# Performance work log

Hardware: AMD Instinct MI355X
Metric: run time of the kernel (lower is better)

## Reference

```python
import jax, jax.numpy as jnp
import numpy as np

B, T, S, H, NUM_HEAD = 4, 1024, 1024, 1024, 16
CAUSAL = True
EPS = 1e-5            # torch nn.LayerNorm default
NEG = -float(2 ** 32)  # masked_fill value in the source


def setup_inputs() -> dict:
    key = jax.random.key(0)
    ks = jax.random.split(key, 8)
    queries = jax.random.normal(ks[0], (B, T, H), jnp.float32)
    keys = jax.random.normal(ks[1], (B, S, H), jnp.float32)
    queries_mask = jax.random.randint(ks[2], (B, T, 1), 0, 2).astype(jnp.int32)
    keys_mask = jax.random.randint(ks[3], (B, S, 1), 0, 2).astype(jnp.int32)
    Wq = jax.random.normal(ks[4], (H, H), jnp.float32) * 0.02
    Wk = jax.random.normal(ks[5], (H, H), jnp.float32) * 0.02
    Wv = jax.random.normal(ks[6], (H, H), jnp.float32) * 0.02
    bq = jnp.zeros((H,), jnp.float32)
    bk = jnp.zeros((H,), jnp.float32)
    bv = jnp.zeros((H,), jnp.float32)
    gamma = jnp.ones((H,), jnp.float32)
    beta = jnp.zeros((H,), jnp.float32)
    return {"queries": queries, "queries_mask": queries_mask, "keys": keys,
            "keys_mask": keys_mask, "Wq": Wq, "bq": bq, "Wk": Wk, "bk": bk,
            "Wv": Wv, "bv": bv, "gamma": gamma, "beta": beta}


def _layernorm(x, gamma, beta):
    m = jnp.mean(x, axis=-1, keepdims=True)
    v = jnp.mean((x - m) ** 2, axis=-1, keepdims=True)  # biased var, as torch
    return gamma * (x - m) / jnp.sqrt(v + EPS) + beta


def reference(queries, queries_mask, keys, keys_mask, Wq, bq, Wk, bk, Wv, bv, gamma, beta):
    dh = H // NUM_HEAD
    # ReLU-activated QKV projections (torch Linear: x @ W.T + b)
    Q = jax.nn.relu(queries @ Wq.T + bq)            # (B,T,H)
    K = jax.nn.relu(keys @ Wk.T + bk)               # (B,S,H)
    V = jax.nn.relu(keys @ Wv.T + bv)               # (B,S,H)
    # chunk along feature dim then cat along batch == (h, B, L, dh) layout
    Qh = Q.reshape(B, T, NUM_HEAD, dh).transpose(2, 0, 1, 3)
    Kh = K.reshape(B, S, NUM_HEAD, dh).transpose(2, 0, 1, 3)
    Vh = V.reshape(B, S, NUM_HEAD, dh).transpose(2, 0, 1, 3)
    # scaled by sqrt(hidden_size), NOT sqrt(head_dim) — faithful to source
    scores = jnp.einsum('hbtd,hbsd->hbts', Qh, Kh) / float(np.sqrt(H))
    # padding mask via outer product of the two masks
    qm = queries_mask[..., 0].astype(jnp.float32)   # (B,T)
    km = keys_mask[..., 0].astype(jnp.float32)      # (B,S)
    pad = (qm[:, :, None] * km[:, None, :]) == 0.0  # (B,T,S) True -> masked
    scores = jnp.where(pad[None], NEG, scores)
    if CAUSAL:
        tri = jnp.triu(jnp.ones((T, S), bool), k=1)  # triu(ones)-eye == strict upper
        scores = jnp.where(tri[None, None], NEG, scores)
    attn = jax.nn.softmax(scores, axis=-1)
    out = jnp.einsum('hbts,hbsd->hbtd', attn, Vh)   # (h,B,T,dh)
    out = out.transpose(1, 2, 0, 3).reshape(B, T, H)  # cat heads back on feature dim
    out = out * queries_mask.astype(jnp.float32)
    return _layernorm(out + queries, gamma, beta)
```

## Files before the change

kernel.cpp:

```cpp
#include <hip/hip_runtime.h>
#include <hip/hip_bf16.h>
#include <math.h>

#define B_ 4
#define T_ 1024
#define S_ 1024
#define H_ 1024
#define NH_ 16
#define DH_ 64
#define NEGV -4294967296.0f
#define EPS_ 1e-5f

typedef __attribute__((ext_vector_type(8))) short short8;
typedef __attribute__((ext_vector_type(8))) unsigned short ushort8;
typedef __attribute__((ext_vector_type(4))) unsigned short ushort4v;
typedef __attribute__((ext_vector_type(4))) unsigned int uint4v;
typedef __attribute__((ext_vector_type(4))) float f32x4;

__device__ __forceinline__ unsigned short f2bf(float x) {
    unsigned int u = __float_as_uint(x);
    u += 0x7FFF + ((u >> 16) & 1);
    return (unsigned short)(u >> 16);
}

__device__ __forceinline__ float bf2f(unsigned short u) {
    return __uint_as_float(((unsigned int)u) << 16);
}

__device__ __forceinline__ unsigned int pack_bf16(float a, float b) {
    union { __hip_bfloat162 h; unsigned int u; } cv;
    cv.h = __float22bfloat162_rn(float2{a, b});
    return cv.u;
}

__device__ __forceinline__ void gload16(const unsigned short* g, unsigned short* l) {
    __builtin_amdgcn_global_load_lds(
        (const __attribute__((address_space(1))) unsigned int*)g,
        (__attribute__((address_space(3))) unsigned int*)l,
        16, 0, 0);
}

#define VMCNT(n) asm volatile("s_waitcnt vmcnt(" #n ")" ::: "memory")
#define LGKM0()  { asm volatile("s_waitcnt lgkmcnt(0)" ::: "memory"); \
                   __builtin_amdgcn_sched_barrier(0); }

__global__ __launch_bounds__(256) void cast_bf16(
    const float* __restrict__ q, const float* __restrict__ k,
    const float* __restrict__ wq, const float* __restrict__ wk,
    const float* __restrict__ wv,
    unsigned short* __restrict__ dq, unsigned short* __restrict__ dk,
    unsigned short* __restrict__ dwq, unsigned short* __restrict__ dwk,
    unsigned short* __restrict__ dwv)
{
    const int seg = blockIdx.y;
    const float* src; unsigned short* dst; int n;
    switch (seg) {
        case 0:  src = q;  dst = dq;  n = B_*T_*H_; break;
        case 1:  src = k;  dst = dk;  n = B_*S_*H_; break;
        case 2:  src = wq; dst = dwq; n = H_*H_;    break;
        case 3:  src = wk; dst = dwk; n = H_*H_;    break;
        default: src = wv; dst = dwv; n = H_*H_;    break;
    }
    const int i = (blockIdx.x * 256 + threadIdx.x) * 8;
    if (i >= n) return;
    float4 a = *(const float4*)&src[i];
    float4 b = *(const float4*)&src[i + 4];
    ushort8 o;
    o[0] = f2bf(a.x); o[1] = f2bf(a.y); o[2] = f2bf(a.z); o[3] = f2bf(a.w);
    o[4] = f2bf(b.x); o[5] = f2bf(b.y); o[6] = f2bf(b.z); o[7] = f2bf(b.w);
    *(ushort8*)&dst[i] = o;
}

template<int MH, int NH>
__device__ __forceinline__ void mfmaQ(f32x4 (&acc)[8][4],
                                      const short8 (&afr)[4][2],
                                      const short8 (&bfr)[2][2])
{
    #pragma unroll
    for (int i2 = 0; i2 < 4; ++i2)
        #pragma unroll
        for (int j2 = 0; j2 < 2; ++j2)
            #pragma unroll
            for (int kc = 0; kc < 2; ++kc)
                acc[MH*4+i2][NH*2+j2] = __builtin_amdgcn_mfma_f32_16x16x32_bf16(
                    afr[i2][kc], bfr[j2][kc], acc[MH*4+i2][NH*2+j2], 0, 0, 0);
}

__global__ __launch_bounds__(512) void qkv_mfma(
    const unsigned short* __restrict__ Xq, const unsigned short* __restrict__ Xk,
    const unsigned short* __restrict__ Wq, const unsigned short* __restrict__ Wk,
    const unsigned short* __restrict__ Wv,
    const float* __restrict__ bq, const float* __restrict__ bk,
    const float* __restrict__ bv,
    unsigned short* __restrict__ Qo, unsigned short* __restrict__ Ko,
    unsigned short* __restrict__ Vo)
{
    const int bi = (blockIdx.x & 7) * 24 + (blockIdx.x >> 3);
    const int col_t = bi >> 4, row_t = bi & 15;
    const int which = col_t >> 2;
    const int colW = (col_t & 3) * 256;
    const int row0 = row_t * 256;

    const unsigned short* X = (which == 0) ? Xq : Xk;
    const unsigned short* Wm = (which == 0) ? Wq : (which == 1) ? Wk : Wv;
    const float* bias        = (which == 0) ? bq : (which == 1) ? bk : bv;
    unsigned short* Out      = (which == 0) ? Qo : (which == 1) ? Ko : Vo;

    __shared__ __align__(16) unsigned short S[67584];

    const int tid = threadIdx.x;
    const int wid = tid >> 6, lane = tid & 63, lo = lane & 15, hi = lane >> 4;
    const int wm = wid >> 2, wn = wid & 3;
    const int swr = (lo & 7) << 3;
    const int csw = ((tid & 7) << 3) ^ (((tid >> 3) & 7) << 3);

    auto stageA = [&](int mh, int kt) {
        const int k0 = kt << 6;
        unsigned short* dst = &S[(kt & 1) * 32768 + mh * 8192 + wid * 512];
        #pragma unroll
        for (int u = 0; u < 2; ++u) {
            const int rowT = row0 + u * 128 + mh * 64 + (tid >> 3);
            gload16(&X[(size_t)rowT * H_ + k0 + csw], dst + u * 4096);
        }
    };
    auto stageB = [&](int nh, int kt) {
        const int k0 = kt << 6;
        unsigned short* dst = &S[(kt & 1) * 32768 + 16384 + nh * 8192 + wid * 512];
        #pragma unroll
        for (int u = 0; u < 2; ++u) {
            const int pr = u * 64 + (tid >> 3);
            const int n  = (pr >> 5) * 64 + nh * 32 + (pr & 31);
            gload16(&Wm[(size_t)(colW + n) * H_ + k0 + csw], dst + u * 4096);
        }
    };

    short8 afr[4][2], blo[2][2], bhi[2][2];
    f32x4 acc[8][4] = {};

    auto readA = [&](int boff, int mh) {
        #pragma unroll
        for (int i2 = 0; i2 < 4; ++i2)
            #pragma unroll
            for (int kc = 0; kc < 2; ++kc)
                afr[i2][kc] = *(const short8*)
                    &S[boff + mh*8192 + (wm*64 + i2*16 + lo)*64 + ((kc*32 + hi*8) ^ swr)];
    };
    auto readB = [&](int boff, int nh, short8 (&bf)[2][2]) {
        #pragma unroll
        for (int j2 = 0; j2 < 2; ++j2)
            #pragma unroll
            for (int kc = 0; kc < 2; ++kc)
                bf[j2][kc] = *(const short8*)
                    &S[boff + 16384 + nh*8192 + (wn*32 + j2*16 + lo)*64 + ((kc*32 + hi*8) ^ swr)];
    };

    stageA(0, 0); stageB(0, 0); stageA(1, 0); stageB(1, 0);
    stageA(0, 1); stageB(0, 1); stageA(1, 1); stageB(1, 1);
    VMCNT(0);
    __builtin_amdgcn_s_barrier();

    for (int it = 0; it < 16; ++it) {
        const int boff = (it & 1) * 32768;
        readA(boff, 0);
        readB(boff, 0, blo);
        if (it >= 1 && it <= 14) stageB(1, it + 1);
        LGKM0();
        __builtin_amdgcn_s_setprio(1); mfmaQ<0,0>(acc, afr, blo); __builtin_amdgcn_s_setprio(0);
        readB(boff, 1, bhi);
        if (it >= 1 && it <= 14) stageA(1, it + 1);
        LGKM0();
        __builtin_amdgcn_s_setprio(1); mfmaQ<0,1>(acc, afr, bhi); __builtin_amdgcn_s_setprio(0);
        readA(boff, 1);
        if (it <= 13) { stageA(0, it + 2); stageB(0, it + 2); }
        __builtin_amdgcn_s_barrier();
        LGKM0();
        __builtin_amdgcn_s_setprio(1);
        mfmaQ<1,0>(acc, afr, blo);
        mfmaQ<1,1>(acc, afr, bhi);
        __builtin_amdgcn_s_setprio(0);
        if (it < 14) { VMCNT(4); } else { VMCNT(0); }
        __builtin_amdgcn_s_barrier();
    }

    float bj[4];
    #pragma unroll
    for (int j = 0; j < 4; ++j)
        bj[j] = bias[colW + wn*64 + (j>>1)*32 + (j&1)*16 + lo];

    #pragma unroll
    for (int i = 0; i < 8; ++i) {
        const int er = wm*128 + (i>>2)*64 + (i&3)*16 + hi*4;
        #pragma unroll
        for (int j = 0; j < 4; ++j) {
            const int ec = wn*64 + (j>>1)*32 + (j&1)*16 + lo;
            #pragma unroll
            for (int r = 0; r < 4; ++r)
                S[(er + r) * 264 + ec] = f2bf(fmaxf(acc[i][j][r] + bj[j], 0.f));
        }
    }
    __syncthreads();
    #pragma unroll
    for (int u = 0; u < 16; ++u) {
        const int cid = u * 512 + tid;
        const int rr = cid >> 5, ch = cid & 31;
        ushort8 v = *(const ushort8*)&S[rr * 264 + ch * 8];
        *(ushort8*)&Out[(size_t)(row0 + rr) * H_ + colW + ch * 8] = v;
    }
}

__global__ __launch_bounds__(256) void vmean_prep(
    const unsigned short* __restrict__ V, const int* __restrict__ kmask,
    float* __restrict__ vmean_part, int* __restrict__ sfirst)
{
    const int bh = blockIdx.x >> 2, chunk = blockIdx.x & 3;
    const int b = bh >> 4, h = bh & 15;
    const int tid = threadIdx.x;
    const int d8 = tid & 7, sg = tid >> 3;

    __shared__ float red[32][68];
    __shared__ int sf_sh;
    if (tid == 0) sf_sh = S_;

    float acc[8] = {0,0,0,0,0,0,0,0};
    #pragma unroll
    for (int it = 0; it < 8; ++it) {
        const int s = chunk * 256 + sg + it * 32;
        ushort8 v = *(const ushort8*)&V[((size_t)b*S_ + s) * H_ + h*DH_ + d8*8];
        #pragma unroll
        for (int i = 0; i < 8; ++i) acc[i] += bf2f(v[i]);
    }
    #pragma unroll
    for (int i = 0; i < 8; ++i) red[sg][d8*8 + i] = acc[i];

    if (blockIdx.x < B_) {
        int lf = S_;
        #pragma unroll
        for (int u = 0; u < 4; ++u) {
            const int s = tid + u * 256;
            if (kmask[blockIdx.x * S_ + s] != 0) lf = min(lf, s);
        }
        atomicMin(&sf_sh, lf);
    }
    __syncthreads();

    for (int str = 16; str >= 1; str >>= 1) {
        if (sg < str) {
            #pragma unroll
            for (int i = 0; i < 8; ++i)
                red[sg][d8*8 + i] += red[sg + str][d8*8 + i];
        }
        __syncthreads();
    }
    if (tid < 64) vmean_part[blockIdx.x * 64 + tid] = red[0][tid] * (1.f / 1024.f);
    if (blockIdx.x < B_ && tid == 0) sfirst[blockIdx.x] = sf_sh;
}

__global__ __launch_bounds__(256) void attn_mfma(
    const unsigned short* __restrict__ Q, const unsigned short* __restrict__ K,
    const unsigned short* __restrict__ V, const int* __restrict__ kmask,
    const float* __restrict__ vmean_part, const int* __restrict__ sfirst,
    unsigned short* __restrict__ Ob)
{
    const int flat = blockIdx.x;
    const int nf = (flat & 7) * 64 + (flat >> 3);
    const int z = nf & 7, bh = nf >> 3;
    const int b = bh >> 4, h = bh & 15;

    const int tid = threadIdx.x;
    const int wid = tid >> 6, lane = tid & 63, hi = lane >> 4, lo = lane & 15;

    __shared__ unsigned short Ks[2][64][64];
    __shared__ unsigned short Vt[2][64][64];

    const int s_first = sfirst[b];

    const int srow = tid >> 2, d0k = (tid & 3) << 4, swk = (srow & 7) << 3;
    const int sp = tid & 31, dg = tid >> 5;
    const int s2 = sp * 2;
    const int ps = (s2 & 35) | ((s2 & 16) >> 2) | ((s2 & 12) << 1);

    ushort8 krA0, krA1, vrA0, vrA1; int kmA;
    ushort8 krB0, krB1, vrB0, vrB1; int kmB;

    auto stage_load = [&](int s0_, ushort8& k0, ushort8& k1,
                          ushort8& v0, ushort8& v1, int& kmr) {
        const unsigned short* kp = &K[((size_t)b*S_ + s0_ + srow) * H_ + h*DH_ + d0k];
        k0 = *(const ushort8*)kp;
        k1 = *(const ushort8*)(kp + 8);
        const unsigned short* vp = &V[((size_t)b*S_ + s0_ + s2) * H_ + h*DH_ + dg*8];
        v0 = *(const ushort8*)vp;
        v1 = *(const ushort8*)(vp + H_);
        kmr = kmask[b*S_ + s0_ + lane];
    };
    auto stage_write = [&](int pb, const ushort8& k0, const ushort8& k1,
                           const ushort8& v0, const ushort8& v1) {
        *(ushort8*)&Ks[pb][srow][d0k ^ swk]       = k0;
        *(ushort8*)&Ks[pb][srow][(d0k + 8) ^ swk] = k1;
        #pragma unroll
        for (int i = 0; i < 8; ++i) {
            const int d = dg*8 + i;
            const unsigned int pk = (unsigned int)(unsigned short)v0[i]
                                  | ((unsigned int)(unsigned short)v1[i] << 16);
            *(unsigned int*)&Vt[pb][d][ps ^ ((d & 7) << 3)] = pk;
        }
    };

    for (int item = 0; item < 2; ++item) {
        const int qt = item ? z : (15 - z);
        const int t0 = qt * 64;
        const int ntiles = qt + 1;
        const int tq = t0 + wid*16 + lo;

        short8 qf0, qf1;
        {
            const unsigned short* qp =
                &Q[((size_t)b*T_ + t0 + wid*16 + lo) * H_ + h*DH_ + hi*8];
            qf0 = *(const short8*)qp;
            qf1 = *(const short8*)(qp + 32);
        }

        float m = -INFINITY, l = 0.f;
        f32x4 oacc[4] = {{0,0,0,0},{0,0,0,0},{0,0,0,0},{0,0,0,0}};

        auto compute = [&](int pb, int s0, int kmr) {
            const unsigned long long kmb = __ballot(kmr != 0);
            f32x4 sc[4] = {{0,0,0,0},{0,0,0,0},{0,0,0,0},{0,0,0,0}};
            const int swq = (lo & 7) << 3;
            __builtin_amdgcn_s_setprio(1);
            #pragma unroll
            for (int n = 0; n < 4; ++n) {
                short8 kfa = *(const short8*)&Ks[pb][n*16 + lo][(hi*8) ^ swq];
                sc[n] = __builtin_amdgcn_mfma_f32_16x16x32_bf16(kfa, qf0, sc[n], 0, 0, 0);
                short8 kfb = *(const short8*)&Ks[pb][n*16 + lo][(32 + hi*8) ^ swq];
                sc[n] = __builtin_amdgcn_mfma_f32_16x16x32_bf16(kfb, qf1, sc[n], 0, 0, 0);
            }
            __builtin_amdgcn_s_setprio(0);
            float p[4][4];
            float rm = -INFINITY;
            #pragma unroll
            for (int n = 0; n < 4; ++n)
                #pragma unroll
                for (int r = 0; r < 4; ++r) {
                    const int sl = n*16 + hi*4 + r;
                    const bool msk = !((kmb >> sl) & 1ull) || (s0 + sl > tq);
                    const float v = sc[n][r] * 0.03125f;
                    p[n][r] = msk ? NEGV : v;
                    rm = fmaxf(rm, p[n][r]);
                }
            rm = fmaxf(rm, __shfl_xor(rm, 16));
            rm = fmaxf(rm, __shfl_xor(rm, 32));
            if (__any(rm > m + 8.f)) {
                const float mn  = fmaxf(m, rm);
                const float scl = __expf(m - mn);
                m = mn;
                l *= scl;
                #pragma unroll
                for (int r = 0; r < 4; ++r) {
                    const float os = __shfl(scl, hi*4 + r);
                    oacc[0][r] *= os; oacc[1][r] *= os;
                    oacc[2][r] *= os; oacc[3][r] *= os;
                }
            }
            float ts = 0.f;
            #pragma unroll
            for (int n = 0; n < 4; ++n)
                #pragma unroll
                for (int r = 0; r < 4; ++r) {
                    p[n][r] = __expf(p[n][r] - m);
                    ts += p[n][r];
                }
            ts += __shfl_xor(ts, 16);
            ts += __shfl_xor(ts, 32);
            l += ts;
            unsigned int pk0[4], pk1[4];
            #pragma unroll
            for (int n = 0; n < 4; ++n) {
                pk0[n] = pack_bf16(p[n][0], p[n][1]);
                pk1[n] = pack_bf16(p[n][2], p[n][3]);
            }
            __builtin_amdgcn_s_setprio(1);
            #pragma unroll
            for (int cch = 0; cch < 2; ++cch) {
                uint4v u;
                u.x = pk0[2*cch];   u.y = pk1[2*cch];
                u.z = pk0[2*cch+1]; u.w = pk1[2*cch+1];
                const short8 pf = __builtin_bit_cast(short8, u);
                #pragma unroll
                for (int n2 = 0; n2 < 4; ++n2) {
                    const int d = n2*16 + lo;
                    const short8 vf =
                        *(const short8*)&Vt[pb][d][(cch*32 + hi*8) ^ ((d & 7) << 3)];
                    oacc[n2] = __builtin_amdgcn_mfma_f32_16x16x32_bf16(pf, vf, oacc[n2], 0, 0, 0);
                }
            }
            __builtin_amdgcn_s_setprio(0);
        };

        __syncthreads();
        stage_load(0, krA0, krA1, vrA0, vrA1, kmA);
        int t = 0;
        for (;;) {
            stage_write(0, krA0, krA1, vrA0, vrA1);
            if (t + 1 < ntiles) stage_load((t+1) << 6, krB0, krB1, vrB0, vrB1, kmB);
            __syncthreads();
            compute(0, t << 6, kmA);
            if (++t >= ntiles) break;

            stage_write(1, krB0, krB1, vrB0, vrB1);
            if (t + 1 < ntiles) stage_load((t+1) << 6, krA0, krA1, vrA0, vrA1, kmA);
            __syncthreads();
            compute(1, t << 6, kmB);
            if (++t >= ntiles) break;
        }

        const float inv = 1.0f / l;
        #pragma unroll
        for (int r = 0; r < 4; ++r) {
            const float ir = __shfl(inv, hi*4 + r);
            const int trow = t0 + wid*16 + hi*4 + r;
            unsigned short* dst = &Ob[((size_t)b*T_ + trow) * H_ + h*DH_ + lo];
            if (trow < s_first) {
                #pragma unroll
                for (int g = 0; g < 4; ++g) {
                    float vm = vmean_part[(bh*4 + 0)*64 + lo + g*16]
                             + vmean_part[(bh*4 + 1)*64 + lo + g*16]
                             + vmean_part[(bh*4 + 2)*64 + lo + g*16]
                             + vmean_part[(bh*4 + 3)*64 + lo + g*16];
                    dst[g*16] = f2bf(vm);
                }
            } else {
                dst[0]  = f2bf(oacc[0][r] * ir);
                dst[16] = f2bf(oacc[1][r] * ir);
                dst[32] = f2bf(oacc[2][r] * ir);
                dst[48] = f2bf(oacc[3][r] * ir);
            }
        }
    }
}

__global__ __launch_bounds__(256) void ln_kernel(
    const unsigned short* __restrict__ Ob, float* __restrict__ Out,
    const float* __restrict__ queries, const int* __restrict__ qmask,
    const float* __restrict__ gamma, const float* __restrict__ beta)
{
    const int row = blockIdx.x;
    const int tid = threadIdx.x;
    const float qm = (float)qmask[row];

    ushort4v a4 = *(const ushort4v*)&Ob[(size_t)row * H_ + tid*4];
    float4 q4 = *(const float4*)&queries[(size_t)row * H_ + tid*4];
    float x0 = bf2f(a4.x) * qm + q4.x;
    float x1 = bf2f(a4.y) * qm + q4.y;
    float x2 = bf2f(a4.z) * qm + q4.z;
    float x3 = bf2f(a4.w) * qm + q4.w;

    float sum = x0 + x1 + x2 + x3;
    float sq  = x0*x0 + x1*x1 + x2*x2 + x3*x3;
    #pragma unroll
    for (int off = 32; off >= 1; off >>= 1) {
        sum += __shfl_down(sum, off);
        sq  += __shfl_down(sq,  off);
    }
    __shared__ float rs[4], rq[4];
    const int wid = tid >> 6, lane = tid & 63;
    if (lane == 0) { rs[wid] = sum; rq[wid] = sq; }
    __syncthreads();
    const float tot  = rs[0] + rs[1] + rs[2] + rs[3];
    const float totq = rq[0] + rq[1] + rq[2] + rq[3];
    const float mean = tot * (1.f / H_);
    const float var  = totq * (1.f / H_) - mean * mean;
    const float rstd = rsqrtf(var + EPS_);

    float4 g4 = *(const float4*)&gamma[tid*4];
    float4 b4 = *(const float4*)&beta[tid*4];
    float4 y;
    y.x = (x0 - mean) * rstd * g4.x + b4.x;
    y.y = (x1 - mean) * rstd * g4.y + b4.y;
    y.z = (x2 - mean) * rstd * g4.z + b4.z;
    y.w = (x3 - mean) * rstd * g4.w + b4.w;
    *(float4*)&Out[(size_t)row * H_ + tid*4] = y;
}

extern "C" void kernel_launch(void* const* d_in, const int* in_sizes, int n_in,
                              void* d_out, int out_size, void* d_ws, size_t ws_size,
                              hipStream_t stream)
{
    const float* queries = (const float*)d_in[0];
    const int*   qmask   = (const int*)  d_in[1];
    const float* keys    = (const float*)d_in[2];
    const int*   kmask   = (const int*)  d_in[3];
    const float* Wq      = (const float*)d_in[4];
    const float* bq      = (const float*)d_in[5];
    const float* Wk      = (const float*)d_in[6];
    const float* bk      = (const float*)d_in[7];
    const float* Wv      = (const float*)d_in[8];
    const float* bv      = (const float*)d_in[9];
    const float* gamma   = (const float*)d_in[10];
    const float* beta    = (const float*)d_in[11];
    float* out = (float*)d_out;

    unsigned short* Xqb = (unsigned short*)d_ws;
    unsigned short* Xkb = Xqb + (size_t)B_*T_*H_;
    unsigned short* Wqb = Xkb + (size_t)B_*S_*H_;
    unsigned short* Wkb = Wqb + (size_t)H_*H_;
    unsigned short* Wvb = Wkb + (size_t)H_*H_;
    unsigned short* Qb  = Wvb + (size_t)H_*H_;
    unsigned short* Kb  = Qb  + (size_t)B_*T_*H_;
    unsigned short* Vb  = Kb  + (size_t)B_*S_*H_;
    float* vmeanF = (float*)Xqb;
    int*   sfirstI = (int*)(vmeanF + 256*64);
    unsigned short* Ob = Xkb;

    dim3 gc((B_*T_*H_/8 + 255)/256, 5, 1);
    cast_bf16<<<gc, 256, 0, stream>>>(queries, keys, Wq, Wk, Wv,
                                      Xqb, Xkb, Wqb, Wkb, Wvb);

    qkv_mfma<<<192, 512, 0, stream>>>(Xqb, Xkb, Wqb, Wkb, Wvb,
                                      bq, bk, bv, Qb, Kb, Vb);

    vmean_prep<<<256, 256, 0, stream>>>(Vb, kmask, vmeanF, sfirstI);

    attn_mfma<<<512, 256, 0, stream>>>(Qb, Kb, Vb, kmask, vmeanF, sfirstI, Ob);

    ln_kernel<<<B_*T_, 256, 0, stream>>>(Ob, out, queries, qmask, gamma, beta);
}
```

Measured before the change: 92.32 us.

## Shrink QKV GEMM tiles to 128x128 for more blocks and occupancy

The QKV projection GEMM now uses 128x128 output tiles per 512-thread block instead of 256x256, so it launches 768 blocks instead of 192 and the shared-memory footprint drops to 64 KB. The per-iteration pipeline is simplified to a single read phase, then a barrier, then the prefetch of k-tile it+2, then one MFMA burst. Launch bounds request 4 blocks per CU. The aim is better CU fill on a 256-CU part, since 192 blocks left CUs idle. The trade-off is lower arithmetic intensity per tile, which means more global and L2 traffic for reloading X and W, and less overlap of LDS reads with MFMAs.

```diff
diff --git a/kernel.cpp b/kernel.cpp
--- a/kernel.cpp
+++ b/kernel.cpp
@@ -71,22 +71,7 @@
     *(ushort8*)&dst[i] = o;
 }
 
-template<int MH, int NH>
-__device__ __forceinline__ void mfmaQ(f32x4 (&acc)[8][4],
-                                      const short8 (&afr)[4][2],
-                                      const short8 (&bfr)[2][2])
-{
-    #pragma unroll
-    for (int i2 = 0; i2 < 4; ++i2)
-        #pragma unroll
-        for (int j2 = 0; j2 < 2; ++j2)
-            #pragma unroll
-            for (int kc = 0; kc < 2; ++kc)
-                acc[MH*4+i2][NH*2+j2] = __builtin_amdgcn_mfma_f32_16x16x32_bf16(
-                    afr[i2][kc], bfr[j2][kc], acc[MH*4+i2][NH*2+j2], 0, 0, 0);
-}
-
-__global__ __launch_bounds__(512) void qkv_mfma(
+__global__ __launch_bounds__(512, 4) void qkv_mfma(
     const unsigned short* __restrict__ Xq, const unsigned short* __restrict__ Xk,
     const unsigned short* __restrict__ Wq, const unsigned short* __restrict__ Wk,
     const unsigned short* __restrict__ Wv,
@@ -95,18 +80,18 @@
     unsigned short* __restrict__ Qo, unsigned short* __restrict__ Ko,
     unsigned short* __restrict__ Vo)
 {
-    const int bi = (blockIdx.x & 7) * 24 + (blockIdx.x >> 3);
-    const int col_t = bi >> 4, row_t = bi & 15;
-    const int which = col_t >> 2;
-    const int colW = (col_t & 3) * 256;
-    const int row0 = row_t * 256;
+    const int bi = (blockIdx.x & 7) * 96 + (blockIdx.x >> 3);
+    const int col_t = bi >> 5, row_t = bi & 31;
+    const int which = col_t >> 3;
+    const int colW = (col_t & 7) * 128;
+    const int row0 = row_t * 128;
 
     const unsigned short* X = (which == 0) ? Xq : Xk;
     const unsigned short* Wm = (which == 0) ? Wq : (which == 1) ? Wk : Wv;
     const float* bias        = (which == 0) ? bq : (which == 1) ? bk : bv;
     unsigned short* Out      = (which == 0) ? Qo : (which == 1) ? Ko : Vo;
 
-    __shared__ __align__(16) unsigned short S[67584];
+    __shared__ __align__(16) unsigned short S[32768];
 
     const int tid = threadIdx.x;
     const int wid = tid >> 6, lane = tid & 63, lo = lane & 15, hi = lane >> 4;
@@ -114,96 +99,92 @@
     const int swr = (lo & 7) << 3;
     const int csw = ((tid & 7) << 3) ^ (((tid >> 3) & 7) << 3);
 
-    auto stageA = [&](int mh, int kt) {
+    auto stageA = [&](int kt) {
         const int k0 = kt << 6;
-        unsigned short* dst = &S[(kt & 1) * 32768 + mh * 8192 + wid * 512];
+        unsigned short* dst = &S[(kt & 1) * 16384 + wid * 512];
         #pragma unroll
         for (int u = 0; u < 2; ++u) {
-            const int rowT = row0 + u * 128 + mh * 64 + (tid >> 3);
+            const int rowT = row0 + u * 64 + (tid >> 3);
             gload16(&X[(size_t)rowT * H_ + k0 + csw], dst + u * 4096);
         }
     };
-    auto stageB = [&](int nh, int kt) {
+    auto stageB = [&](int kt) {
         const int k0 = kt << 6;
-        unsigned short* dst = &S[(kt & 1) * 32768 + 16384 + nh * 8192 + wid * 512];
+        unsigned short* dst = &S[(kt & 1) * 16384 + 8192 + wid * 512];
         #pragma unroll
         for (int u = 0; u < 2; ++u) {
-            const int pr = u * 64 + (tid >> 3);
-            const int n  = (pr >> 5) * 64 + nh * 32 + (pr & 31);
+            const int n = u * 64 + (tid >> 3);
             gload16(&Wm[(size_t)(colW + n) * H_ + k0 + csw], dst + u * 4096);
         }
     };
 
-    short8 afr[4][2], blo[2][2], bhi[2][2];
-    f32x4 acc[8][4] = {};
-
-    auto readA = [&](int boff, int mh) {
+    short8 afr[4][2], bfr[2][2];
+    f32x4 acc[4][2] = {};
+
+    auto readA = [&](int boff) {
         #pragma unroll
         for (int i2 = 0; i2 < 4; ++i2)
             #pragma unroll
             for (int kc = 0; kc < 2; ++kc)
                 afr[i2][kc] = *(const short8*)
-                    &S[boff + mh*8192 + (wm*64 + i2*16 + lo)*64 + ((kc*32 + hi*8) ^ swr)];
+                    &S[boff + (wm*64 + i2*16 + lo)*64 + ((kc*32 + hi*8) ^ swr)];
     };
-    auto readB = [&](int boff, int nh, short8 (&bf)[2][2]) {
+    auto readB = [&](int boff) {
         #pragma unroll
         for (int j2 = 0; j2 < 2; ++j2)
             #pragma unroll
             for (int kc = 0; kc < 2; ++kc)
-                bf[j2][kc] = *(const short8*)
-                    &S[boff + 16384 + nh*8192 + (wn*32 + j2*16 + lo)*64 + ((kc*32 + hi*8) ^ swr)];
+                bfr[j2][kc] = *(const short8*)
+                    &S[boff + 8192 + (wn*32 + j2*16 + lo)*64 + ((kc*32 + hi*8) ^ swr)];
     };
 
-    stageA(0, 0); stageB(0, 0); stageA(1, 0); stageB(1, 0);
-    stageA(0, 1); stageB(0, 1); stageA(1, 1); stageB(1, 1);
-    VMCNT(0);
+    float bj[2];
+    #pragma unroll
+    for (int j2 = 0; j2 < 2; ++j2)
+        bj[j2] = bias[colW + wn*32 + j2*16 + lo];
+
+    stageA(0); stageB(0); stageA(1); stageB(1);
+    VMCNT(4);
     __builtin_amdgcn_s_barrier();
 
     for (int it = 0; it < 16; ++it) {
-        const int boff = (it & 1) * 32768;
-        readA(boff, 0);
-        readB(boff, 0, blo);
-        if (it >= 1 && it <= 14) stageB(1, it + 1);
+        const int boff = (it & 1) * 16384;
+        readA(boff);
+        readB(boff);
         LGKM0();
-        __builtin_amdgcn_s_setprio(1); mfmaQ<0,0>(acc, afr, blo); __builtin_amdgcn_s_setprio(0);
-        readB(boff, 1, bhi);
-        if (it >= 1 && it <= 14) stageA(1, it + 1);
-        LGKM0();
-        __builtin_amdgcn_s_setprio(1); mfmaQ<0,1>(acc, afr, bhi); __builtin_amdgcn_s_setprio(0);
-        readA(boff, 1);
-        if (it <= 13) { stageA(0, it + 2); stageB(0, it + 2); }
         __builtin_amdgcn_s_barrier();
-        LGKM0();
+        if (it <= 13) { stageA(it + 2); stageB(it + 2); }
         __builtin_amdgcn_s_setprio(1);
-        mfmaQ<1,0>(acc, afr, blo);
-        mfmaQ<1,1>(acc, afr, bhi);
+        #pragma unroll
+        for (int i2 = 0; i2 < 4; ++i2)
+            #pragma unroll
+            for (int j2 = 0; j2 < 2; ++j2)
+                #pragma unroll
+                for (int kc = 0; kc < 2; ++kc)
+                    acc[i2][j2] = __builtin_amdgcn_mfma_f32_16x16x32_bf16(
+                        afr[i2][kc], bfr[j2][kc], acc[i2][j2], 0, 0, 0);
         __builtin_amdgcn_s_setprio(0);
         if (it < 14) { VMCNT(4); } else { VMCNT(0); }
         __builtin_amdgcn_s_barrier();
     }
 
-    float bj[4];
     #pragma unroll
-    for (int j = 0; j < 4; ++j)
-        bj[j] = bias[colW + wn*64 + (j>>1)*32 + (j&1)*16 + lo];
-
-    #pragma unroll
-    for (int i = 0; i < 8; ++i) {
-        const int er = wm*128 + (i>>2)*64 + (i&3)*16 + hi*4;
-        #pragma unroll
-        for (int j = 0; j < 4; ++j) {
-            const int ec = wn*64 + (j>>1)*32 + (j&1)*16 + lo;
+    for (int i2 = 0; i2 < 4; ++i2) {
+        const int er = wm*64 + i2*16 + hi*4;
+        #pragma unroll
+        for (int j2 = 0; j2 < 2; ++j2) {
+            const int ec = wn*32 + j2*16 + lo;
             #pragma unroll
             for (int r = 0; r < 4; ++r)
-                S[(er + r) * 264 + ec] = f2bf(fmaxf(acc[i][j][r] + bj[j], 0.f));
+                S[(er + r) * 136 + ec] = f2bf(fmaxf(acc[i2][j2][r] + bj[j2], 0.f));
         }
     }
     __syncthreads();
     #pragma unroll
-    for (int u = 0; u < 16; ++u) {
+    for (int u = 0; u < 4; ++u) {
         const int cid = u * 512 + tid;
-        const int rr = cid >> 5, ch = cid & 31;
-        ushort8 v = *(const ushort8*)&S[rr * 264 + ch * 8];
+        const int rr = cid >> 4, ch = cid & 15;
+        ushort8 v = *(const ushort8*)&S[rr * 136 + ch * 8];
         *(ushort8*)&Out[(size_t)(row0 + rr) * H_ + colW + ch * 8] = v;
     }
 }
@@ -515,7 +496,7 @@
     cast_bf16<<<gc, 256, 0, stream>>>(queries, keys, Wq, Wk, Wv,
                                       Xqb, Xkb, Wqb, Wkb, Wvb);
 
-    qkv_mfma<<<192, 512, 0, stream>>>(Xqb, Xkb, Wqb, Wkb, Wvb,
+    qkv_mfma<<<768, 512, 0, stream>>>(Xqb, Xkb, Wqb, Wkb, Wvb,
                                       bq, bk, bv, Qb, Kb, Vb);
 
     vmean_prep<<<256, 256, 0, stream>>>(Vb, kmask, vmeanF, sfirstI);
```

Result: no change. 92.32 us (-0.0%).
